# Kernel optimization log

Measured on AMD Instinct MI355X. Metric: run time of the kernel, lower is better.

## Reference

```python
import jax, jax.numpy as jnp
import numpy as np

N_NODES = 100000
N_EDGES = 1600000
FEATURE = 32
HIDDEN = 64
CLASSES = 10
K = 3  # TAGConv default number of hops


def setup_inputs() -> dict:
    key = jax.random.key(0)
    k1, k2, k3, k4, k5, k6, k7 = jax.random.split(key, 7)
    x = jax.random.normal(k1, (N_NODES, FEATURE), dtype=jnp.float32)
    edge_index = jax.random.randint(k2, (2, N_EDGES), 0, N_NODES, dtype=jnp.int32)
    # TAGConv holds K+1 linear maps (one per hop power) plus a bias.
    s1 = 1.0 / np.sqrt(FEATURE)
    s2 = 1.0 / np.sqrt(HIDDEN)
    W1 = jax.random.uniform(k3, (K + 1, FEATURE, HIDDEN), jnp.float32, -s1, s1)
    b1 = jax.random.uniform(k4, (HIDDEN,), jnp.float32, -s1, s1)
    W2 = jax.random.uniform(k5, (K + 1, HIDDEN, CLASSES), jnp.float32, -s2, s2)
    b2 = jax.random.uniform(k6, (CLASSES,), jnp.float32, -s2, s2)
    return {"x": x, "edge_index": edge_index, "W1": W1, "b1": b1, "W2": W2, "b2": b2}


def _tagconv(x, row, col, norm, W, b):
    # out = sum_k (A_hat^k x) W_k + b, A_hat = D^-1/2 A D^-1/2 (no self loops)
    out = x @ W[0]
    h = x
    for k in range(1, W.shape[0]):
        h = jnp.zeros_like(h).at[col].add(norm[:, None] * h[row])
        out = out + h @ W[k]
    return out + b


def reference(x, edge_index, W1, b1, W2, b2):
    row, col = edge_index[0], edge_index[1]
    n = x.shape[0]
    # gcn_norm with unit edge weights, add_self_loops=False
    deg = jnp.zeros((n,), x.dtype).at[col].add(1.0)
    dinv = jnp.where(deg > 0, jax.lax.rsqrt(jnp.maximum(deg, 1.0)), 0.0)
    norm = dinv[row] * dinv[col]

    h = _tagconv(x, row, col, norm, W1, b1)
    h = jax.nn.relu(h)
    # dropout is identity in eval mode
    h = _tagconv(h, row, col, norm, W2, b2)
    return jax.nn.log_softmax(h, axis=1)
```

## Files before the change

### kernel.cpp

```cpp
#include <hip/hip_runtime.h>

typedef unsigned int uint;
typedef unsigned short ushort_t;
typedef short s8v __attribute__((ext_vector_type(8)));
typedef float f4v __attribute__((ext_vector_type(4)));

#define N_NODES 100000
#define N_EDGES 1600000
#define FEAT 32
#define HID 64
#define NCLS 10

#define BUCKET_SHIFT 8
#define NBUCKET 391
#define NCB 256
#define CHUNK ((N_EDGES + NCB - 1) / NCB)
#define BH_N (NBUCKET * NCB)
#define NB_BH ((BH_N + 255) / 256)
#define CAP 6144
#define LROW 65

#define G32_BLOCKS 6144
#define G16_BLOCKS 3072


__device__ __forceinline__ uint pack_bf16(float lo, float hi) {
    uint a = __float_as_uint(lo);
    uint b = __float_as_uint(hi);
    a = a + 0x7fffu + ((a >> 16) & 1u);
    b = b + 0x7fffu + ((b >> 16) & 1u);
    return (a >> 16) | (b & 0xffff0000u);
}
__device__ __forceinline__ float unp_lo(uint v) { return __uint_as_float(v << 16); }
__device__ __forceinline__ float unp_hi(uint v) { return __uint_as_float(v & 0xffff0000u); }

__device__ __forceinline__ s8v to_s8(uint4 u) {
    union { uint4 u; s8v s; } x;
    x.u = u;
    return x.s;
}


__global__ void bucket_hist(const int* __restrict__ col, int* __restrict__ blockhist) {
    __shared__ int lh[NBUCKET];
    int blk = blockIdx.x;
    for (int i = threadIdx.x; i < NBUCKET; i += 256) lh[i] = 0;
    __syncthreads();
    int e0 = blk * CHUNK;
    int e1 = min(e0 + CHUNK, N_EDGES);
    for (int e = e0 + threadIdx.x; e < e1; e += 256)
        atomicAdd(&lh[col[e] >> BUCKET_SHIFT], 1);
    __syncthreads();
    for (int i = threadIdx.x; i < NBUCKET; i += 256)
        blockhist[i * NCB + blk] = lh[i];
}

__global__ void scanA_kernel(const int* __restrict__ src, int* __restrict__ dst,
                             int* __restrict__ bsum, int n) {
    __shared__ int s[256];
    int gid = blockIdx.x * 256 + threadIdx.x;
    int v = (gid < n) ? src[gid] : 0;
    s[threadIdx.x] = v;
    __syncthreads();
    for (int off = 1; off < 256; off <<= 1) {
        int t = (threadIdx.x >= off) ? s[threadIdx.x - off] : 0;
        __syncthreads();
        s[threadIdx.x] += t;
        __syncthreads();
    }
    if (gid < n) dst[gid] = s[threadIdx.x] - v;
    if (threadIdx.x == 255) bsum[blockIdx.x] = s[255];
}

__global__ void scanB_kernel(int* __restrict__ bsum, int nb) {
    __shared__ int s[512];
    int v = (threadIdx.x < nb) ? bsum[threadIdx.x] : 0;
    s[threadIdx.x] = v;
    __syncthreads();
    for (int off = 1; off < 512; off <<= 1) {
        int t = (threadIdx.x >= off) ? s[threadIdx.x - off] : 0;
        __syncthreads();
        s[threadIdx.x] += t;
        __syncthreads();
    }
    if (threadIdx.x < nb) bsum[threadIdx.x] = s[threadIdx.x] - v;
}

__global__ void scanC_add(int* __restrict__ dst, const int* __restrict__ bsum, int n) {
    int gid = blockIdx.x * 256 + threadIdx.x;
    if (gid < n) dst[gid] += bsum[blockIdx.x];
}

__global__ void bucket_scatter(const int* __restrict__ row, const int* __restrict__ col,
                               const int* __restrict__ base, int* __restrict__ packed) {
    __shared__ int lcnt[NBUCKET];
    __shared__ int lbase[NBUCKET];
    int blk = blockIdx.x;
    for (int i = threadIdx.x; i < NBUCKET; i += 256) {
        lcnt[i] = 0;
        lbase[i] = base[i * NCB + blk];
    }
    __syncthreads();
    int e0 = blk * CHUNK;
    int e1 = min(e0 + CHUNK, N_EDGES);
    for (int e = e0 + threadIdx.x; e < e1; e += 256) {
        int c = col[e];
        int r = row[e];
        int b = c >> BUCKET_SHIFT;
        int pos = lbase[b] + atomicAdd(&lcnt[b], 1);
        packed[pos] = (r << BUCKET_SHIFT) | (c & 255);
    }
}

__global__ void bucket_sort(const int* __restrict__ base, const int* __restrict__ packed,
                            int* __restrict__ rowptr, ushort_t* __restrict__ elo,
                            ushort_t* __restrict__ nmid, float* __restrict__ dinv) {
    __shared__ int stage[CAP];
    __shared__ int cnt[512];
    __shared__ int excl[512];
    __shared__ int psum[256];
    int b = blockIdx.x;
    int tid = threadIdx.x;
    int s = base[b * NCB];
    int e = (b == NBUCKET - 1) ? N_EDGES : base[(b + 1) * NCB];
    int m = e - s;
    cnt[tid] = 0;
    cnt[tid + 256] = 0;
    __syncthreads();
    for (int i = tid; i < m; i += 256) {
        int p = packed[s + i];
        if (i < CAP) stage[i] = p;
        int r = p >> BUCKET_SHIFT;
        int key = ((p & 255) << 1) | (r >= 65536);
        atomicAdd(&cnt[key], 1);
    }
    __syncthreads();
    int c0 = cnt[2 * tid], c1 = cnt[2 * tid + 1];
    psum[tid] = c0 + c1;
    __syncthreads();
    for (int off = 1; off < 256; off <<= 1) {
        int t = (tid >= off) ? psum[tid - off] : 0;
        __syncthreads();
        psum[tid] += t;
        __syncthreads();
    }
    int tot = c0 + c1;
    int pex = psum[tid] - tot;
    excl[2 * tid] = pex;
    excl[2 * tid + 1] = pex + c0;
    int node = (b << BUCKET_SHIFT) + tid;
    if (node < N_NODES) {
        dinv[node] = (tot > 0) ? rsqrtf((float)tot) : 0.0f;
        rowptr[node] = s + pex;
        nmid[node] = (ushort_t)c0;
    }
    if (b == NBUCKET - 1 && tid == 0) rowptr[N_NODES] = N_EDGES;
    __syncthreads();
    cnt[tid] = 0;
    cnt[tid + 256] = 0;
    __syncthreads();
    for (int i = tid; i < m; i += 256) {
        int p = (i < CAP) ? stage[i] : packed[s + i];
        int r = p >> BUCKET_SHIFT;
        int key = ((p & 255) << 1) | (r >= 65536);
        int pos = excl[key] + atomicAdd(&cnt[key], 1);
        elo[s + pos] = (ushort_t)r;
    }
}


__global__ void prescale_kernel(const float* __restrict__ x, const float* __restrict__ dinv,
                                uint* __restrict__ t0) {
    int i = blockIdx.x * 256 + threadIdx.x;
    if (i < N_NODES * 16) {
        int node = i >> 4, fp = i & 15;
        float dv = dinv[node];
        t0[i] = pack_bf16(x[node * 32 + 2 * fp] * dv, x[node * 32 + 2 * fp + 1] * dv);
    }
}


template <int WP>
__global__ void gather32_kernel(const int* __restrict__ rowptr, const ushort_t* __restrict__ elo,
                                const ushort_t* __restrict__ nmid,
                                const float* __restrict__ dinv, const uint* __restrict__ src,
                                uint* __restrict__ pout, uint* __restrict__ preout) {
    int wid = (blockIdx.x * 256 + threadIdx.x) >> 6;
    int lane = threadIdx.x & 63;
    int fp = lane & 15;
    int g = lane >> 4;
    const int NW = G32_BLOCKS * 4;
    for (int node = wid; node < N_NODES; node += NW) {
        int s = rowptr[node], e = rowptr[node + 1];
        int smid = s + nmid[node];
        float acc0 = 0.0f, acc1 = 0.0f;
        int base = (s & ~3) + g * 4;
        for (int b = base; b < e; b += 16) {
            ushort4 q = *(const ushort4*)(elo + b);
            int i0 = q.x | ((b     >= smid) ? 0x10000 : 0);
            int i1 = q.y | ((b + 1 >= smid) ? 0x10000 : 0);
            int i2 = q.z | ((b + 2 >= smid) ? 0x10000 : 0);
            int i3 = q.w | ((b + 3 >= smid) ? 0x10000 : 0);
            uint v0 = (b     >= s && b     < e) ? src[i0 * 16 + fp] : 0u;
            uint v1 = (b + 1 >= s && b + 1 < e) ? src[i1 * 16 + fp] : 0u;
            uint v2 = (b + 2 >= s && b + 2 < e) ? src[i2 * 16 + fp] : 0u;
            uint v3 = (b + 3 >= s && b + 3 < e) ? src[i3 * 16 + fp] : 0u;
            acc0 += unp_lo(v0) + unp_lo(v1) + unp_lo(v2) + unp_lo(v3);
            acc1 += unp_hi(v0) + unp_hi(v1) + unp_hi(v2) + unp_hi(v3);
        }
        acc0 += __shfl_xor(acc0, 16);
        acc0 += __shfl_xor(acc0, 32);
        acc1 += __shfl_xor(acc1, 16);
        acc1 += __shfl_xor(acc1, 32);
        if (lane < 16) {
            float dv = dinv[node];
            pout[node * 16 + fp] = pack_bf16(dv * acc0, dv * acc1);
            if (WP) {
                float d2 = dv * dv;
                preout[node * 16 + fp] = pack_bf16(d2 * acc0, d2 * acc1);
            }
        }
    }
}

template <int FINAL>
__global__ void gather16_kernel(const int* __restrict__ rowptr, const ushort_t* __restrict__ elo,
                                const ushort_t* __restrict__ nmid,
                                const float* __restrict__ dinv, const uint* __restrict__ src,
                                const uint* __restrict__ add, void* __restrict__ outv) {
    int wid = (blockIdx.x * 256 + threadIdx.x) >> 6;
    int lane = threadIdx.x & 63;
    int fp = lane & 7;
    int g = (lane >> 3) & 3;
    int half = lane >> 5;
    const int NW = G16_BLOCKS * 4;
    const int NPAIR = N_NODES / 2;
    for (int p = wid; p < NPAIR; p += NW) {
        int node = p * 2 + half;
        int s = rowptr[node], e = rowptr[node + 1];
        int smid = s + nmid[node];
        float acc0 = 0.0f, acc1 = 0.0f;
        int base = (s & ~3) + g * 4;
        for (int b = base; b < e; b += 16) {
            ushort4 q = *(const ushort4*)(elo + b);
            int i0 = q.x | ((b     >= smid) ? 0x10000 : 0);
            int i1 = q.y | ((b + 1 >= smid) ? 0x10000 : 0);
            int i2 = q.z | ((b + 2 >= smid) ? 0x10000 : 0);
            int i3 = q.w | ((b + 3 >= smid) ? 0x10000 : 0);
            uint v0 = (b     >= s && b     < e) ? src[i0 * 8 + fp] : 0u;
            uint v1 = (b + 1 >= s && b + 1 < e) ? src[i1 * 8 + fp] : 0u;
            uint v2 = (b + 2 >= s && b + 2 < e) ? src[i2 * 8 + fp] : 0u;
            uint v3 = (b + 3 >= s && b + 3 < e) ? src[i3 * 8 + fp] : 0u;
            acc0 += unp_lo(v0) + unp_lo(v1) + unp_lo(v2) + unp_lo(v3);
            acc1 += unp_hi(v0) + unp_hi(v1) + unp_hi(v2) + unp_hi(v3);
        }
        acc0 += __shfl_xor(acc0, 8);
        acc0 += __shfl_xor(acc0, 16);
        acc1 += __shfl_xor(acc1, 8);
        acc1 += __shfl_xor(acc1, 16);
        float dv = dinv[node];
        uint av = add[node * 8 + fp];
        float v0 = unp_lo(av) + dv * acc0;
        float v1 = unp_hi(av) + dv * acc1;
        if (!FINAL) {
            if (g == 0) ((uint*)outv)[node * 8 + fp] = pack_bf16(dv * v0, dv * v1);
        } else {
            float l0 = (2 * fp     < NCLS) ? v0 : -1e30f;
            float l1 = (2 * fp + 1 < NCLS) ? v1 : -1e30f;
            float m = fmaxf(l0, l1);
            m = fmaxf(m, __shfl_xor(m, 1));
            m = fmaxf(m, __shfl_xor(m, 2));
            m = fmaxf(m, __shfl_xor(m, 4));
            float ex = ((2 * fp     < NCLS) ? __expf(l0 - m) : 0.0f)
                     + ((2 * fp + 1 < NCLS) ? __expf(l1 - m) : 0.0f);
            ex += __shfl_xor(ex, 1);
            ex += __shfl_xor(ex, 2);
            ex += __shfl_xor(ex, 4);
            float ls = logf(ex) + m;
            if (g == 0 && fp < 5) {
                float2 o = {l0 - ls, l1 - ls};
                *(float2*)((float*)outv + (size_t)node * 10 + 2 * fp) = o;
            }
        }
    }
}


__global__ void wfprep_kernel(const float* __restrict__ W1, const float* __restrict__ W2,
                              uint* __restrict__ wf1, uint* __restrict__ wf2) {
    int idx = blockIdx.x * 256 + threadIdx.x;
    if (idx < 4096) {
        int vj = idx & 3, frag = idx >> 2;
        int lane = frag & 63, ks = (frag >> 6) & 3, nt = frag >> 8;
        int g = lane >> 4, c = lane & 15;
        int k0 = ks * 32 + g * 8 + 2 * vj;
        int n = nt * 16 + c;
        wf1[idx] = pack_bf16(W1[k0 * 64 + n], W1[(k0 + 1) * 64 + n]);
    } else if (idx < 6144) {
        int i2 = idx - 4096;
        int vj = i2 & 3, frag = i2 >> 2;
        int lane = frag & 63, ks = (frag >> 6) & 1, nt = frag >> 7;
        int g = lane >> 4, c = lane & 15;
        int k0 = ks * 32 + g * 8 + 2 * vj;
        float v0 = (c < NCLS) ? W2[(nt * HID + k0) * NCLS + c] : 0.0f;
        float v1 = (c < NCLS) ? W2[(nt * HID + k0 + 1) * NCLS + c] : 0.0f;
        wf2[i2] = pack_bf16(v0, v1);
    }
}


__global__ __launch_bounds__(256) void dense_fused(
        const float* __restrict__ x, const uint* __restrict__ p1,
        const uint* __restrict__ p2, const uint* __restrict__ p3,
        const uint* __restrict__ wf1, const uint* __restrict__ wf2,
        const float* __restrict__ b1, const float* __restrict__ b2,
        const float* __restrict__ dinv, uint* __restrict__ z, int zstride) {
    __shared__ float hls[4 * 16 * LROW];
    int tid = threadIdx.x;
    int wv = tid >> 6, l = tid & 63, g = l >> 4, c = l & 15;
    float* my = hls + wv * 16 * LROW;
    int row0 = blockIdx.x * 64 + wv * 16;
    int ra = row0 + c;
    int rc = min(ra, N_NODES - 1);

    uint4 au0;
    {
        float4 xa = *(const float4*)(x + rc * 32 + g * 8);
        float4 xb = *(const float4*)(x + rc * 32 + g * 8 + 4);
        au0.x = pack_bf16(xa.x, xa.y);
        au0.y = pack_bf16(xa.z, xa.w);
        au0.z = pack_bf16(xb.x, xb.y);
        au0.w = pack_bf16(xb.z, xb.w);
    }
    uint4 au1 = *(const uint4*)(p1 + rc * 16 + g * 4);
    uint4 au2 = *(const uint4*)(p2 + rc * 16 + g * 4);
    uint4 au3 = *(const uint4*)(p3 + rc * 16 + g * 4);
    s8v a0 = to_s8(au0), a1 = to_s8(au1), a2 = to_s8(au2), a3 = to_s8(au3);

    f4v acc[4];
#pragma unroll
    for (int nt = 0; nt < 4; nt++) {
        f4v ac = {0.f, 0.f, 0.f, 0.f};
        const s8v* wp = (const s8v*)(wf1 + (nt * 4) * 64 * 4 + l * 4);
        ac = __builtin_amdgcn_mfma_f32_16x16x32_bf16(a0, wp[0 * 64], ac, 0, 0, 0);
        ac = __builtin_amdgcn_mfma_f32_16x16x32_bf16(a1, wp[1 * 64], ac, 0, 0, 0);
        ac = __builtin_amdgcn_mfma_f32_16x16x32_bf16(a2, wp[2 * 64], ac, 0, 0, 0);
        ac = __builtin_amdgcn_mfma_f32_16x16x32_bf16(a3, wp[3 * 64], ac, 0, 0, 0);
        acc[nt] = ac;
    }

#pragma unroll
    for (int nt = 0; nt < 4; nt++) {
        float bb = b1[nt * 16 + c];
#pragma unroll
        for (int reg = 0; reg < 4; reg++) {
            my[(4 * g + reg) * LROW + nt * 16 + c] = fmaxf(acc[nt][reg] + bb, 0.0f);
        }
    }
    __syncthreads();

    uint4 b2u[2];
#pragma unroll
    for (int ks = 0; ks < 2; ks++) {
        float4 h0 = *(const float4*)&my[c * LROW + ks * 32 + g * 8];
        float4 h1 = *(const float4*)&my[c * LROW + ks * 32 + g * 8 + 4];
        b2u[ks].x = pack_bf16(h0.x, h0.y);
        b2u[ks].y = pack_bf16(h0.z, h0.w);
        b2u[ks].z = pack_bf16(h1.x, h1.y);
        b2u[ks].w = pack_bf16(h1.z, h1.w);
    }
    s8v h0f = to_s8(b2u[0]), h1f = to_s8(b2u[1]);

    f4v acc2[4];
#pragma unroll
    for (int nt = 0; nt < 4; nt++) {
        f4v ac = {0.f, 0.f, 0.f, 0.f};
        const s8v* wp = (const s8v*)(wf2 + (nt * 2) * 64 * 4 + l * 4);
        ac = __builtin_amdgcn_mfma_f32_16x16x32_bf16(h0f, wp[0 * 64], ac, 0, 0, 0);
        ac = __builtin_amdgcn_mfma_f32_16x16x32_bf16(h1f, wp[1 * 64], ac, 0, 0, 0);
        acc2[nt] = ac;
    }

#pragma unroll
    for (int nt = 0; nt < 4; nt++) {
        float bb = (nt == 0 && c < NCLS) ? b2[c] : 0.0f;
        uint* zk = z + (size_t)nt * zstride;
#pragma unroll
        for (int reg = 0; reg < 4; reg++) {
            int rr = row0 + 4 * g + reg;
            float v = acc2[nt][reg] + bb;
            if (nt == 3) v *= dinv[min(rr, N_NODES - 1)];
            float vn = __shfl_xor(v, 1);
            if (rr < N_NODES && (c & 1) == 0) {
                zk[rr * 8 + (c >> 1)] = pack_bf16(v, vn);
            }
        }
    }
}


extern "C" void kernel_launch(void* const* d_in, const int* in_sizes, int n_in,
                              void* d_out, int out_size, void* d_ws, size_t ws_size,
                              hipStream_t stream) {
    const float* x  = (const float*)d_in[0];
    const int*   ei = (const int*)d_in[1];
    const float* W1 = (const float*)d_in[2];
    const float* b1 = (const float*)d_in[3];
    const float* W2 = (const float*)d_in[4];
    const float* b2 = (const float*)d_in[5];
    float* out = (float*)d_out;

    const int* row = ei;
    const int* col = ei + N_EDGES;

    float* w = (float*)d_ws;
    size_t o = 0;
    auto alloc = [&](size_t nel) { float* p = w + o; o += (nel + 63) & ~(size_t)63; return p; };

    int*      rowptr = (int*)alloc(N_NODES + 1);
    int*      bsum   = (int*)alloc(512);
    float*    dinv   = alloc(N_NODES);
    ushort_t* nmid   = (ushort_t*)alloc(50048);
    uint*     wf1    = (uint*)alloc(4096);
    uint*     wf2    = (uint*)alloc(2048);
    ushort_t* elo    = (ushort_t*)alloc(800064);
    float*    bufA   = alloc((size_t)N_NODES * 32);
    float*    bufB   = alloc((size_t)N_NODES * 32);
    float*    bufC   = alloc((size_t)N_NODES * 32);
    float*    bufD   = alloc((size_t)N_NODES * 32);
    float*    h      = alloc((size_t)N_NODES * HID);

    int* blockhist = (int*)bufB;
    int* bhbase    = (int*)bufC;
    int* packed    = (int*)h;

    uint* t0  = (uint*)bufA;
    uint* p1  = (uint*)bufB;
    uint* p1p = (uint*)bufC;
    uint* p2  = (uint*)bufD;
    uint* p2p = (uint*)bufA;
    uint* p3  = (uint*)bufC;
    const int ZS = N_NODES * 8;
    uint* z0  = (uint*)h;
    uint* z1  = (uint*)h + ZS;
    uint* z2  = (uint*)h + 2 * (size_t)ZS;
    uint* z3p = (uint*)h + 3 * (size_t)ZS;
    uint* tAp = (uint*)bufC;
    uint* tBp = (uint*)bufC + ZS;

    const int TB = 256;

    bucket_hist<<<NCB, TB, 0, stream>>>(col, blockhist);
    scanA_kernel<<<NB_BH, TB, 0, stream>>>(blockhist, bhbase, bsum, BH_N);
    scanB_kernel<<<1, 512, 0, stream>>>(bsum, NB_BH);
    scanC_add<<<NB_BH, TB, 0, stream>>>(bhbase, bsum, BH_N);
    bucket_scatter<<<NCB, TB, 0, stream>>>(row, col, bhbase, packed);
    bucket_sort<<<NBUCKET, TB, 0, stream>>>(bhbase, packed, rowptr, elo, nmid, dinv);

    wfprep_kernel<<<24, TB, 0, stream>>>(W1, W2, wf1, wf2);

    prescale_kernel<<<(N_NODES * 16 + TB - 1) / TB, TB, 0, stream>>>(x, dinv, t0);
    gather32_kernel<1><<<G32_BLOCKS, TB, 0, stream>>>(rowptr, elo, nmid, dinv, t0,  p1, p1p);
    gather32_kernel<1><<<G32_BLOCKS, TB, 0, stream>>>(rowptr, elo, nmid, dinv, p1p, p2, p2p);
    gather32_kernel<0><<<G32_BLOCKS, TB, 0, stream>>>(rowptr, elo, nmid, dinv, p2p, p3, nullptr);

    int gF = (N_NODES + 63) / 64;
    dense_fused<<<gF, TB, 0, stream>>>(x, p1, p2, p3, wf1, wf2, b1, b2, dinv, z0, ZS);

    gather16_kernel<0><<<G16_BLOCKS, TB, 0, stream>>>(rowptr, elo, nmid, dinv, z3p, z2, tAp);
    gather16_kernel<0><<<G16_BLOCKS, TB, 0, stream>>>(rowptr, elo, nmid, dinv, tAp, z1, tBp);
    gather16_kernel<1><<<G16_BLOCKS, TB, 0, stream>>>(rowptr, elo, nmid, dinv, tBp, z0, out);
}
```

Measured before the change: 291.0 us.

## Split 10-class buffers into 4+1 word planes and launch one wave per node

```diff
diff --git a/kernel.cpp b/kernel.cpp
--- a/kernel.cpp
+++ b/kernel.cpp
@@ -19,9 +19,6 @@
 #define NB_BH ((BH_N + 255) / 256)
 #define CAP 6144
 #define LROW 65
-
-#define G32_BLOCKS 6144
-#define G16_BLOCKS 3072
 
 
 __device__ __forceinline__ uint pack_bf16(float lo, float hi) {
@@ -185,40 +182,38 @@
                                 const ushort_t* __restrict__ nmid,
                                 const float* __restrict__ dinv, const uint* __restrict__ src,
                                 uint* __restrict__ pout, uint* __restrict__ preout) {
-    int wid = (blockIdx.x * 256 + threadIdx.x) >> 6;
+    int node = (blockIdx.x * blockDim.x + threadIdx.x) >> 6;
+    if (node >= N_NODES) return;
     int lane = threadIdx.x & 63;
     int fp = lane & 15;
     int g = lane >> 4;
-    const int NW = G32_BLOCKS * 4;
-    for (int node = wid; node < N_NODES; node += NW) {
-        int s = rowptr[node], e = rowptr[node + 1];
-        int smid = s + nmid[node];
-        float acc0 = 0.0f, acc1 = 0.0f;
-        int base = (s & ~3) + g * 4;
-        for (int b = base; b < e; b += 16) {
-            ushort4 q = *(const ushort4*)(elo + b);
-            int i0 = q.x | ((b     >= smid) ? 0x10000 : 0);
-            int i1 = q.y | ((b + 1 >= smid) ? 0x10000 : 0);
-            int i2 = q.z | ((b + 2 >= smid) ? 0x10000 : 0);
-            int i3 = q.w | ((b + 3 >= smid) ? 0x10000 : 0);
-            uint v0 = (b     >= s && b     < e) ? src[i0 * 16 + fp] : 0u;
-            uint v1 = (b + 1 >= s && b + 1 < e) ? src[i1 * 16 + fp] : 0u;
-            uint v2 = (b + 2 >= s && b + 2 < e) ? src[i2 * 16 + fp] : 0u;
-            uint v3 = (b + 3 >= s && b + 3 < e) ? src[i3 * 16 + fp] : 0u;
-            acc0 += unp_lo(v0) + unp_lo(v1) + unp_lo(v2) + unp_lo(v3);
-            acc1 += unp_hi(v0) + unp_hi(v1) + unp_hi(v2) + unp_hi(v3);
-        }
-        acc0 += __shfl_xor(acc0, 16);
-        acc0 += __shfl_xor(acc0, 32);
-        acc1 += __shfl_xor(acc1, 16);
-        acc1 += __shfl_xor(acc1, 32);
-        if (lane < 16) {
-            float dv = dinv[node];
-            pout[node * 16 + fp] = pack_bf16(dv * acc0, dv * acc1);
-            if (WP) {
-                float d2 = dv * dv;
-                preout[node * 16 + fp] = pack_bf16(d2 * acc0, d2 * acc1);
-            }
+    int s = rowptr[node], e = rowptr[node + 1];
+    int smid = s + nmid[node];
+    float acc0 = 0.0f, acc1 = 0.0f;
+    int base = (s & ~3) + g * 4;
+    for (int b = base; b < e; b += 16) {
+        ushort4 q = *(const ushort4*)(elo + b);
+        int i0 = q.x | ((b     >= smid) ? 0x10000 : 0);
+        int i1 = q.y | ((b + 1 >= smid) ? 0x10000 : 0);
+        int i2 = q.z | ((b + 2 >= smid) ? 0x10000 : 0);
+        int i3 = q.w | ((b + 3 >= smid) ? 0x10000 : 0);
+        uint v0 = (b     >= s && b     < e) ? src[i0 * 16 + fp] : 0u;
+        uint v1 = (b + 1 >= s && b + 1 < e) ? src[i1 * 16 + fp] : 0u;
+        uint v2 = (b + 2 >= s && b + 2 < e) ? src[i2 * 16 + fp] : 0u;
+        uint v3 = (b + 3 >= s && b + 3 < e) ? src[i3 * 16 + fp] : 0u;
+        acc0 += unp_lo(v0) + unp_lo(v1) + unp_lo(v2) + unp_lo(v3);
+        acc1 += unp_hi(v0) + unp_hi(v1) + unp_hi(v2) + unp_hi(v3);
+    }
+    acc0 += __shfl_xor(acc0, 16);
+    acc0 += __shfl_xor(acc0, 32);
+    acc1 += __shfl_xor(acc1, 16);
+    acc1 += __shfl_xor(acc1, 32);
+    if (lane < 16) {
+        float dv = dinv[node];
+        pout[node * 16 + fp] = pack_bf16(dv * acc0, dv * acc1);
+        if (WP) {
+            float d2 = dv * dv;
+            preout[node * 16 + fp] = pack_bf16(d2 * acc0, d2 * acc1);
         }
     }
 }
@@ -226,61 +221,72 @@
 template <int FINAL>
 __global__ void gather16_kernel(const int* __restrict__ rowptr, const ushort_t* __restrict__ elo,
                                 const ushort_t* __restrict__ nmid,
-                                const float* __restrict__ dinv, const uint* __restrict__ src,
-                                const uint* __restrict__ add, void* __restrict__ outv) {
+                                const float* __restrict__ dinv,
+                                const uint* __restrict__ srcA, const uint* __restrict__ srcB,
+                                const uint* __restrict__ addA, const uint* __restrict__ addB,
+                                uint* __restrict__ outA, uint* __restrict__ outB,
+                                float* __restrict__ outF) {
     int wid = (blockIdx.x * 256 + threadIdx.x) >> 6;
     int lane = threadIdx.x & 63;
+    int node = wid * 2 + (lane >> 5);
+    if (node >= N_NODES) return;
     int fp = lane & 7;
     int g = (lane >> 3) & 3;
-    int half = lane >> 5;
-    const int NW = G16_BLOCKS * 4;
-    const int NPAIR = N_NODES / 2;
-    for (int p = wid; p < NPAIR; p += NW) {
-        int node = p * 2 + half;
-        int s = rowptr[node], e = rowptr[node + 1];
-        int smid = s + nmid[node];
-        float acc0 = 0.0f, acc1 = 0.0f;
-        int base = (s & ~3) + g * 4;
-        for (int b = base; b < e; b += 16) {
-            ushort4 q = *(const ushort4*)(elo + b);
-            int i0 = q.x | ((b     >= smid) ? 0x10000 : 0);
-            int i1 = q.y | ((b + 1 >= smid) ? 0x10000 : 0);
-            int i2 = q.z | ((b + 2 >= smid) ? 0x10000 : 0);
-            int i3 = q.w | ((b + 3 >= smid) ? 0x10000 : 0);
-            uint v0 = (b     >= s && b     < e) ? src[i0 * 8 + fp] : 0u;
-            uint v1 = (b + 1 >= s && b + 1 < e) ? src[i1 * 8 + fp] : 0u;
-            uint v2 = (b + 2 >= s && b + 2 < e) ? src[i2 * 8 + fp] : 0u;
-            uint v3 = (b + 3 >= s && b + 3 < e) ? src[i3 * 8 + fp] : 0u;
-            acc0 += unp_lo(v0) + unp_lo(v1) + unp_lo(v2) + unp_lo(v3);
-            acc1 += unp_hi(v0) + unp_hi(v1) + unp_hi(v2) + unp_hi(v3);
-        }
-        acc0 += __shfl_xor(acc0, 8);
-        acc0 += __shfl_xor(acc0, 16);
-        acc1 += __shfl_xor(acc1, 8);
-        acc1 += __shfl_xor(acc1, 16);
-        float dv = dinv[node];
-        uint av = add[node * 8 + fp];
-        float v0 = unp_lo(av) + dv * acc0;
-        float v1 = unp_hi(av) + dv * acc1;
-        if (!FINAL) {
-            if (g == 0) ((uint*)outv)[node * 8 + fp] = pack_bf16(dv * v0, dv * v1);
-        } else {
-            float l0 = (2 * fp     < NCLS) ? v0 : -1e30f;
-            float l1 = (2 * fp + 1 < NCLS) ? v1 : -1e30f;
-            float m = fmaxf(l0, l1);
-            m = fmaxf(m, __shfl_xor(m, 1));
-            m = fmaxf(m, __shfl_xor(m, 2));
-            m = fmaxf(m, __shfl_xor(m, 4));
-            float ex = ((2 * fp     < NCLS) ? __expf(l0 - m) : 0.0f)
-                     + ((2 * fp + 1 < NCLS) ? __expf(l1 - m) : 0.0f);
-            ex += __shfl_xor(ex, 1);
-            ex += __shfl_xor(ex, 2);
-            ex += __shfl_xor(ex, 4);
-            float ls = logf(ex) + m;
-            if (g == 0 && fp < 5) {
-                float2 o = {l0 - ls, l1 - ls};
-                *(float2*)((float*)outv + (size_t)node * 10 + 2 * fp) = o;
-            }
+    int s = rowptr[node], e = rowptr[node + 1];
+    int smid = s + nmid[node];
+    float acc0 = 0.0f, acc1 = 0.0f;
+    int base = (s & ~3) + g * 4;
+    for (int b = base; b < e; b += 16) {
+        ushort4 q = *(const ushort4*)(elo + b);
+        int i0 = q.x | ((b     >= smid) ? 0x10000 : 0);
+        int i1 = q.y | ((b + 1 >= smid) ? 0x10000 : 0);
+        int i2 = q.z | ((b + 2 >= smid) ? 0x10000 : 0);
+        int i3 = q.w | ((b + 3 >= smid) ? 0x10000 : 0);
+        uint v0 = 0u, v1 = 0u, v2 = 0u, v3 = 0u;
+        if (fp < 4) {
+            if (b     >= s && b     < e) v0 = srcA[i0 * 4 + fp];
+            if (b + 1 >= s && b + 1 < e) v1 = srcA[i1 * 4 + fp];
+            if (b + 2 >= s && b + 2 < e) v2 = srcA[i2 * 4 + fp];
+            if (b + 3 >= s && b + 3 < e) v3 = srcA[i3 * 4 + fp];
+        } else if (fp == 4) {
+            if (b     >= s && b     < e) v0 = srcB[i0];
+            if (b + 1 >= s && b + 1 < e) v1 = srcB[i1];
+            if (b + 2 >= s && b + 2 < e) v2 = srcB[i2];
+            if (b + 3 >= s && b + 3 < e) v3 = srcB[i3];
+        }
+        acc0 += unp_lo(v0) + unp_lo(v1) + unp_lo(v2) + unp_lo(v3);
+        acc1 += unp_hi(v0) + unp_hi(v1) + unp_hi(v2) + unp_hi(v3);
+    }
+    acc0 += __shfl_xor(acc0, 8);
+    acc0 += __shfl_xor(acc0, 16);
+    acc1 += __shfl_xor(acc1, 8);
+    acc1 += __shfl_xor(acc1, 16);
+    float dv = dinv[node];
+    uint av = (fp < 4) ? addA[node * 4 + fp] : (fp == 4) ? addB[node] : 0u;
+    float v0 = unp_lo(av) + dv * acc0;
+    float v1 = unp_hi(av) + dv * acc1;
+    if (!FINAL) {
+        if (g == 0) {
+            uint pv = pack_bf16(dv * v0, dv * v1);
+            if (fp < 4) outA[node * 4 + fp] = pv;
+            else if (fp == 4) outB[node] = pv;
+        }
+    } else {
+        float l0 = (2 * fp     < NCLS) ? v0 : -1e30f;
+        float l1 = (2 * fp + 1 < NCLS) ? v1 : -1e30f;
+        float m = fmaxf(l0, l1);
+        m = fmaxf(m, __shfl_xor(m, 1));
+        m = fmaxf(m, __shfl_xor(m, 2));
+        m = fmaxf(m, __shfl_xor(m, 4));
+        float ex = ((2 * fp     < NCLS) ? __expf(l0 - m) : 0.0f)
+                 + ((2 * fp + 1 < NCLS) ? __expf(l1 - m) : 0.0f);
+        ex += __shfl_xor(ex, 1);
+        ex += __shfl_xor(ex, 2);
+        ex += __shfl_xor(ex, 4);
+        float ls = logf(ex) + m;
+        if (g == 0 && fp < 5) {
+            float2 o = {l0 - ls, l1 - ls};
+            *(float2*)(outF + (size_t)node * 10 + 2 * fp) = o;
         }
     }
 }
@@ -314,7 +320,7 @@
         const uint* __restrict__ p2, const uint* __restrict__ p3,
         const uint* __restrict__ wf1, const uint* __restrict__ wf2,
         const float* __restrict__ b1, const float* __restrict__ b2,
-        const float* __restrict__ dinv, uint* __restrict__ z, int zstride) {
+        const float* __restrict__ dinv, uint* __restrict__ zA, uint* __restrict__ zB) {
     __shared__ float hls[4 * 16 * LROW];
     int tid = threadIdx.x;
     int wv = tid >> 6, l = tid & 63, g = l >> 4, c = l & 15;
@@ -384,7 +390,8 @@
 #pragma unroll
     for (int nt = 0; nt < 4; nt++) {
         float bb = (nt == 0 && c < NCLS) ? b2[c] : 0.0f;
-        uint* zk = z + (size_t)nt * zstride;
+        uint* zAk = zA + (size_t)nt * (N_NODES * 4);
+        uint* zBk = zB + (size_t)nt * N_NODES;
 #pragma unroll
         for (int reg = 0; reg < 4; reg++) {
             int rr = row0 + 4 * g + reg;
@@ -392,7 +399,9 @@
             if (nt == 3) v *= dinv[min(rr, N_NODES - 1)];
             float vn = __shfl_xor(v, 1);
             if (rr < N_NODES && (c & 1) == 0) {
-                zk[rr * 8 + (c >> 1)] = pack_bf16(v, vn);
+                uint pv = pack_bf16(v, vn);
+                if (c < 8) zAk[rr * 4 + (c >> 1)] = pv;
+                else if (c == 8) zBk[rr] = pv;
             }
         }
     }
@@ -440,15 +449,18 @@
     uint* p2  = (uint*)bufD;
     uint* p2p = (uint*)bufA;
     uint* p3  = (uint*)bufC;
-    const int ZS = N_NODES * 8;
-    uint* z0  = (uint*)h;
-    uint* z1  = (uint*)h + ZS;
-    uint* z2  = (uint*)h + 2 * (size_t)ZS;
-    uint* z3p = (uint*)h + 3 * (size_t)ZS;
-    uint* tAp = (uint*)bufC;
-    uint* tBp = (uint*)bufC + ZS;
+    uint* zA = (uint*)h;
+    uint* zB = zA + 4 * (size_t)N_NODES * 4;
+    const size_t ZSA = (size_t)N_NODES * 4;
+    const size_t ZSB = N_NODES;
+    uint* tAA = (uint*)bufC;
+    uint* tAB = tAA + N_NODES * 4;
+    uint* tBA = tAB + N_NODES;
+    uint* tBB = tBA + N_NODES * 4;
 
     const int TB = 256;
+    const int gW = (N_NODES * 64) / TB;
+    const int gW2 = ((N_NODES + 1) / 2 * 64 + TB - 1) / TB;
 
     bucket_hist<<<NCB, TB, 0, stream>>>(col, blockhist);
     scanA_kernel<<<NB_BH, TB, 0, stream>>>(blockhist, bhbase, bsum, BH_N);
@@ -460,14 +472,17 @@
     wfprep_kernel<<<24, TB, 0, stream>>>(W1, W2, wf1, wf2);
 
     prescale_kernel<<<(N_NODES * 16 + TB - 1) / TB, TB, 0, stream>>>(x, dinv, t0);
-    gather32_kernel<1><<<G32_BLOCKS, TB, 0, stream>>>(rowptr, elo, nmid, dinv, t0,  p1, p1p);
-    gather32_kernel<1><<<G32_BLOCKS, TB, 0, stream>>>(rowptr, elo, nmid, dinv, p1p, p2, p2p);
-    gather32_kernel<0><<<G32_BLOCKS, TB, 0, stream>>>(rowptr, elo, nmid, dinv, p2p, p3, nullptr);
+    gather32_kernel<1><<<gW, TB, 0, stream>>>(rowptr, elo, nmid, dinv, t0,  p1, p1p);
+    gather32_kernel<1><<<gW, TB, 0, stream>>>(rowptr, elo, nmid, dinv, p1p, p2, p2p);
+    gather32_kernel<0><<<gW, TB, 0, stream>>>(rowptr, elo, nmid, dinv, p2p, p3, nullptr);
 
     int gF = (N_NODES + 63) / 64;
-    dense_fused<<<gF, TB, 0, stream>>>(x, p1, p2, p3, wf1, wf2, b1, b2, dinv, z0, ZS);
-
-    gather16_kernel<0><<<G16_BLOCKS, TB, 0, stream>>>(rowptr, elo, nmid, dinv, z3p, z2, tAp);
-    gather16_kernel<0><<<G16_BLOCKS, TB, 0, stream>>>(rowptr, elo, nmid, dinv, tAp, z1, tBp);
-    gather16_kernel<1><<<G16_BLOCKS, TB, 0, stream>>>(rowptr, elo, nmid, dinv, tBp, z0, out);
-}
+    dense_fused<<<gF, TB, 0, stream>>>(x, p1, p2, p3, wf1, wf2, b1, b2, dinv, zA, zB);
+
+    gather16_kernel<0><<<gW2, TB, 0, stream>>>(rowptr, elo, nmid, dinv,
+        zA + 3 * ZSA, zB + 3 * ZSB, zA + 2 * ZSA, zB + 2 * ZSB, tAA, tAB, nullptr);
+    gather16_kernel<0><<<gW2, TB, 0, stream>>>(rowptr, elo, nmid, dinv,
+        tAA, tAB, zA + 1 * ZSA, zB + 1 * ZSB, tBA, tBB, nullptr);
+    gather16_kernel<1><<<gW2, TB, 0, stream>>>(rowptr, elo, nmid, dinv,
+        tBA, tBB, zA, zB, nullptr, nullptr, out);
+}
```

Result: no change. 296.6 us (+1.9%).

## Split 32-wide gathers into two 16-wide halves with prewarmed L2 and nontemporal IO

Applied to the files above, without the earlier changes.

```diff
diff --git a/kernel.cpp b/kernel.cpp
--- a/kernel.cpp
+++ b/kernel.cpp
@@ -20,8 +20,10 @@
 #define CAP 6144
 #define LROW 65
 
-#define G32_BLOCKS 6144
-#define G16_BLOCKS 3072
+#define GRID_G 2048
+#define NPAIR (N_NODES / 2)
+#define SRCW (N_NODES * 8)
+#define WCHUNK ((SRCW + 255) / 256)
 
 
 __device__ __forceinline__ uint pack_bf16(float lo, float hi) {
@@ -173,68 +175,35 @@
                                 uint* __restrict__ t0) {
     int i = blockIdx.x * 256 + threadIdx.x;
     if (i < N_NODES * 16) {
-        int node = i >> 4, fp = i & 15;
+        int node = i >> 4, fpf = i & 15;
         float dv = dinv[node];
-        t0[i] = pack_bf16(x[node * 32 + 2 * fp] * dv, x[node * 32 + 2 * fp + 1] * dv);
-    }
-}
-
-
-template <int WP>
-__global__ void gather32_kernel(const int* __restrict__ rowptr, const ushort_t* __restrict__ elo,
-                                const ushort_t* __restrict__ nmid,
-                                const float* __restrict__ dinv, const uint* __restrict__ src,
-                                uint* __restrict__ pout, uint* __restrict__ preout) {
-    int wid = (blockIdx.x * 256 + threadIdx.x) >> 6;
+        uint pv = pack_bf16(x[node * 32 + 2 * fpf] * dv, x[node * 32 + 2 * fpf + 1] * dv);
+        t0[(size_t)(fpf >> 3) * SRCW + node * 8 + (fpf & 7)] = pv;
+    }
+}
+
+template <int MODE>
+__global__ __launch_bounds__(256) void gatherH_kernel(
+        const int* __restrict__ rowptr, const ushort_t* __restrict__ elo,
+        const ushort_t* __restrict__ nmid, const float* __restrict__ dinv,
+        const uint* __restrict__ src, const uint* __restrict__ add,
+        uint* __restrict__ out0, uint* __restrict__ out1, float* __restrict__ outF) {
+    {
+        int cid = blockIdx.x >> 3;
+        int a0 = cid * WCHUNK;
+        int a1 = min(a0 + WCHUNK, SRCW);
+        uint d = 0;
+        for (int i = a0 + threadIdx.x; i < a1; i += 256) d += src[i];
+        asm volatile("" :: "v"(d));
+    }
+
     int lane = threadIdx.x & 63;
-    int fp = lane & 15;
-    int g = lane >> 4;
-    const int NW = G32_BLOCKS * 4;
-    for (int node = wid; node < N_NODES; node += NW) {
-        int s = rowptr[node], e = rowptr[node + 1];
-        int smid = s + nmid[node];
-        float acc0 = 0.0f, acc1 = 0.0f;
-        int base = (s & ~3) + g * 4;
-        for (int b = base; b < e; b += 16) {
-            ushort4 q = *(const ushort4*)(elo + b);
-            int i0 = q.x | ((b     >= smid) ? 0x10000 : 0);
-            int i1 = q.y | ((b + 1 >= smid) ? 0x10000 : 0);
-            int i2 = q.z | ((b + 2 >= smid) ? 0x10000 : 0);
-            int i3 = q.w | ((b + 3 >= smid) ? 0x10000 : 0);
-            uint v0 = (b     >= s && b     < e) ? src[i0 * 16 + fp] : 0u;
-            uint v1 = (b + 1 >= s && b + 1 < e) ? src[i1 * 16 + fp] : 0u;
-            uint v2 = (b + 2 >= s && b + 2 < e) ? src[i2 * 16 + fp] : 0u;
-            uint v3 = (b + 3 >= s && b + 3 < e) ? src[i3 * 16 + fp] : 0u;
-            acc0 += unp_lo(v0) + unp_lo(v1) + unp_lo(v2) + unp_lo(v3);
-            acc1 += unp_hi(v0) + unp_hi(v1) + unp_hi(v2) + unp_hi(v3);
-        }
-        acc0 += __shfl_xor(acc0, 16);
-        acc0 += __shfl_xor(acc0, 32);
-        acc1 += __shfl_xor(acc1, 16);
-        acc1 += __shfl_xor(acc1, 32);
-        if (lane < 16) {
-            float dv = dinv[node];
-            pout[node * 16 + fp] = pack_bf16(dv * acc0, dv * acc1);
-            if (WP) {
-                float d2 = dv * dv;
-                preout[node * 16 + fp] = pack_bf16(d2 * acc0, d2 * acc1);
-            }
-        }
-    }
-}
-
-template <int FINAL>
-__global__ void gather16_kernel(const int* __restrict__ rowptr, const ushort_t* __restrict__ elo,
-                                const ushort_t* __restrict__ nmid,
-                                const float* __restrict__ dinv, const uint* __restrict__ src,
-                                const uint* __restrict__ add, void* __restrict__ outv) {
-    int wid = (blockIdx.x * 256 + threadIdx.x) >> 6;
-    int lane = threadIdx.x & 63;
+    int half = lane >> 5;
     int fp = lane & 7;
     int g = (lane >> 3) & 3;
-    int half = lane >> 5;
-    const int NW = G16_BLOCKS * 4;
-    const int NPAIR = N_NODES / 2;
+    int wid = (blockIdx.x * 256 + threadIdx.x) >> 6;
+    const int NW = GRID_G * 4;
+
     for (int p = wid; p < NPAIR; p += NW) {
         int node = p * 2 + half;
         int s = rowptr[node], e = rowptr[node + 1];
@@ -242,11 +211,13 @@
         float acc0 = 0.0f, acc1 = 0.0f;
         int base = (s & ~3) + g * 4;
         for (int b = base; b < e; b += 16) {
-            ushort4 q = *(const ushort4*)(elo + b);
-            int i0 = q.x | ((b     >= smid) ? 0x10000 : 0);
-            int i1 = q.y | ((b + 1 >= smid) ? 0x10000 : 0);
-            int i2 = q.z | ((b + 2 >= smid) ? 0x10000 : 0);
-            int i3 = q.w | ((b + 3 >= smid) ? 0x10000 : 0);
+            const uint* ep = (const uint*)(elo + b);
+            uint e0 = __builtin_nontemporal_load(ep);
+            uint e1 = __builtin_nontemporal_load(ep + 1);
+            int i0 = (int)(e0 & 0xffffu) | ((b     >= smid) ? 0x10000 : 0);
+            int i1 = (int)(e0 >> 16)     | ((b + 1 >= smid) ? 0x10000 : 0);
+            int i2 = (int)(e1 & 0xffffu) | ((b + 2 >= smid) ? 0x10000 : 0);
+            int i3 = (int)(e1 >> 16)     | ((b + 3 >= smid) ? 0x10000 : 0);
             uint v0 = (b     >= s && b     < e) ? src[i0 * 8 + fp] : 0u;
             uint v1 = (b + 1 >= s && b + 1 < e) ? src[i1 * 8 + fp] : 0u;
             uint v2 = (b + 2 >= s && b + 2 < e) ? src[i2 * 8 + fp] : 0u;
@@ -259,27 +230,42 @@
         acc1 += __shfl_xor(acc1, 8);
         acc1 += __shfl_xor(acc1, 16);
         float dv = dinv[node];
-        uint av = add[node * 8 + fp];
-        float v0 = unp_lo(av) + dv * acc0;
-        float v1 = unp_hi(av) + dv * acc1;
-        if (!FINAL) {
-            if (g == 0) ((uint*)outv)[node * 8 + fp] = pack_bf16(dv * v0, dv * v1);
+        if (MODE <= 1) {
+            if (g == 0) {
+                uint pv = pack_bf16(dv * acc0, dv * acc1);
+                __builtin_nontemporal_store(pv, out0 + node * 8 + fp);
+                if (MODE == 0) {
+                    float d2 = dv * dv;
+                    uint qv = pack_bf16(d2 * acc0, d2 * acc1);
+                    __builtin_nontemporal_store(qv, out1 + node * 8 + fp);
+                }
+            }
         } else {
-            float l0 = (2 * fp     < NCLS) ? v0 : -1e30f;
-            float l1 = (2 * fp + 1 < NCLS) ? v1 : -1e30f;
-            float m = fmaxf(l0, l1);
-            m = fmaxf(m, __shfl_xor(m, 1));
-            m = fmaxf(m, __shfl_xor(m, 2));
-            m = fmaxf(m, __shfl_xor(m, 4));
-            float ex = ((2 * fp     < NCLS) ? __expf(l0 - m) : 0.0f)
-                     + ((2 * fp + 1 < NCLS) ? __expf(l1 - m) : 0.0f);
-            ex += __shfl_xor(ex, 1);
-            ex += __shfl_xor(ex, 2);
-            ex += __shfl_xor(ex, 4);
-            float ls = logf(ex) + m;
-            if (g == 0 && fp < 5) {
-                float2 o = {l0 - ls, l1 - ls};
-                *(float2*)((float*)outv + (size_t)node * 10 + 2 * fp) = o;
+            uint av = __builtin_nontemporal_load(add + node * 8 + fp);
+            float v0 = unp_lo(av) + dv * acc0;
+            float v1 = unp_hi(av) + dv * acc1;
+            if (MODE == 2) {
+                if (g == 0) {
+                    uint pv = pack_bf16(dv * v0, dv * v1);
+                    __builtin_nontemporal_store(pv, out0 + node * 8 + fp);
+                }
+            } else {
+                float l0 = (2 * fp     < NCLS) ? v0 : -1e30f;
+                float l1 = (2 * fp + 1 < NCLS) ? v1 : -1e30f;
+                float m = fmaxf(l0, l1);
+                m = fmaxf(m, __shfl_xor(m, 1));
+                m = fmaxf(m, __shfl_xor(m, 2));
+                m = fmaxf(m, __shfl_xor(m, 4));
+                float ex = ((2 * fp     < NCLS) ? __expf(l0 - m) : 0.0f)
+                         + ((2 * fp + 1 < NCLS) ? __expf(l1 - m) : 0.0f);
+                ex += __shfl_xor(ex, 1);
+                ex += __shfl_xor(ex, 2);
+                ex += __shfl_xor(ex, 4);
+                float ls = logf(ex) + m;
+                if (g == 0 && fp < 5) {
+                    float2 o = {l0 - ls, l1 - ls};
+                    *(float2*)(outF + (size_t)node * 10 + 2 * fp) = o;
+                }
             }
         }
     }
@@ -314,7 +300,7 @@
         const uint* __restrict__ p2, const uint* __restrict__ p3,
         const uint* __restrict__ wf1, const uint* __restrict__ wf2,
         const float* __restrict__ b1, const float* __restrict__ b2,
-        const float* __restrict__ dinv, uint* __restrict__ z, int zstride) {
+        const float* __restrict__ dinv, uint* __restrict__ z) {
     __shared__ float hls[4 * 16 * LROW];
     int tid = threadIdx.x;
     int wv = tid >> 6, l = tid & 63, g = l >> 4, c = l & 15;
@@ -323,6 +309,7 @@
     int ra = row0 + c;
     int rc = min(ra, N_NODES - 1);
 
+    size_t hofs = (size_t)(g >> 1) * SRCW + rc * 8 + (g & 1) * 4;
     uint4 au0;
     {
         float4 xa = *(const float4*)(x + rc * 32 + g * 8);
@@ -332,9 +319,9 @@
         au0.z = pack_bf16(xb.x, xb.y);
         au0.w = pack_bf16(xb.z, xb.w);
     }
-    uint4 au1 = *(const uint4*)(p1 + rc * 16 + g * 4);
-    uint4 au2 = *(const uint4*)(p2 + rc * 16 + g * 4);
-    uint4 au3 = *(const uint4*)(p3 + rc * 16 + g * 4);
+    uint4 au1 = *(const uint4*)(p1 + hofs);
+    uint4 au2 = *(const uint4*)(p2 + hofs);
+    uint4 au3 = *(const uint4*)(p3 + hofs);
     s8v a0 = to_s8(au0), a1 = to_s8(au1), a2 = to_s8(au2), a3 = to_s8(au3);
 
     f4v acc[4];
@@ -384,7 +371,7 @@
 #pragma unroll
     for (int nt = 0; nt < 4; nt++) {
         float bb = (nt == 0 && c < NCLS) ? b2[c] : 0.0f;
-        uint* zk = z + (size_t)nt * zstride;
+        uint* zk = z + (size_t)nt * SRCW;
 #pragma unroll
         for (int reg = 0; reg < 4; reg++) {
             int rr = row0 + 4 * g + reg;
@@ -440,13 +427,9 @@
     uint* p2  = (uint*)bufD;
     uint* p2p = (uint*)bufA;
     uint* p3  = (uint*)bufC;
-    const int ZS = N_NODES * 8;
-    uint* z0  = (uint*)h;
-    uint* z1  = (uint*)h + ZS;
-    uint* z2  = (uint*)h + 2 * (size_t)ZS;
-    uint* z3p = (uint*)h + 3 * (size_t)ZS;
-    uint* tAp = (uint*)bufC;
-    uint* tBp = (uint*)bufC + ZS;
+    uint* z  = (uint*)h;
+    uint* tA = (uint*)bufD;
+    uint* tB = (uint*)bufA;
 
     const int TB = 256;
 
@@ -460,14 +443,23 @@
     wfprep_kernel<<<24, TB, 0, stream>>>(W1, W2, wf1, wf2);
 
     prescale_kernel<<<(N_NODES * 16 + TB - 1) / TB, TB, 0, stream>>>(x, dinv, t0);
-    gather32_kernel<1><<<G32_BLOCKS, TB, 0, stream>>>(rowptr, elo, nmid, dinv, t0,  p1, p1p);
-    gather32_kernel<1><<<G32_BLOCKS, TB, 0, stream>>>(rowptr, elo, nmid, dinv, p1p, p2, p2p);
-    gather32_kernel<0><<<G32_BLOCKS, TB, 0, stream>>>(rowptr, elo, nmid, dinv, p2p, p3, nullptr);
+    for (int hh = 0; hh < 2; hh++)
+        gatherH_kernel<0><<<GRID_G, TB, 0, stream>>>(rowptr, elo, nmid, dinv,
+            t0 + hh * (size_t)SRCW, nullptr, p1 + hh * (size_t)SRCW, p1p + hh * (size_t)SRCW, nullptr);
+    for (int hh = 0; hh < 2; hh++)
+        gatherH_kernel<0><<<GRID_G, TB, 0, stream>>>(rowptr, elo, nmid, dinv,
+            p1p + hh * (size_t)SRCW, nullptr, p2 + hh * (size_t)SRCW, p2p + hh * (size_t)SRCW, nullptr);
+    for (int hh = 0; hh < 2; hh++)
+        gatherH_kernel<1><<<GRID_G, TB, 0, stream>>>(rowptr, elo, nmid, dinv,
+            p2p + hh * (size_t)SRCW, nullptr, p3 + hh * (size_t)SRCW, nullptr, nullptr);
 
     int gF = (N_NODES + 63) / 64;
-    dense_fused<<<gF, TB, 0, stream>>>(x, p1, p2, p3, wf1, wf2, b1, b2, dinv, z0, ZS);
-
-    gather16_kernel<0><<<G16_BLOCKS, TB, 0, stream>>>(rowptr, elo, nmid, dinv, z3p, z2, tAp);
-    gather16_kernel<0><<<G16_BLOCKS, TB, 0, stream>>>(rowptr, elo, nmid, dinv, tAp, z1, tBp);
-    gather16_kernel<1><<<G16_BLOCKS, TB, 0, stream>>>(rowptr, elo, nmid, dinv, tBp, z0, out);
-}
+    dense_fused<<<gF, TB, 0, stream>>>(x, p1, p2, p3, wf1, wf2, b1, b2, dinv, z);
+
+    gatherH_kernel<2><<<GRID_G, TB, 0, stream>>>(rowptr, elo, nmid, dinv,
+        z + 3 * (size_t)SRCW, z + 2 * (size_t)SRCW, tA, nullptr, nullptr);
+    gatherH_kernel<2><<<GRID_G, TB, 0, stream>>>(rowptr, elo, nmid, dinv,
+        tA, z + 1 * (size_t)SRCW, tB, nullptr, nullptr);
+    gatherH_kernel<3><<<GRID_G, TB, 0, stream>>>(rowptr, elo, nmid, dinv,
+        tB, z, nullptr, nullptr, out);
+}
```

Result: slower. 358.0 us (+23.0%).
